# Kernel tuning notes

Measured on AMD Instinct MI355X. Metric: run time of the kernel, lower is better.

## Reference

```python
import jax, jax.numpy as jnp
import numpy as np

B, T, C = 2, 2048, 1024
N_HEAD, N_GROUP = 16, 4
N_KV = N_HEAD // N_GROUP          # 4
HEAD_DIM = C // N_HEAD            # 64
ROPE_BASE = 10000.0
INIT_STD = 0.02


def setup_inputs() -> dict:
    key = jax.random.key(0)
    ks = jax.random.split(key, 5)
    kvC = N_KV * HEAD_DIM
    return {
        "x": jax.random.normal(ks[0], (B, T, C), jnp.float32),
        "w_q": jax.random.normal(ks[1], (C, C), jnp.float32) * INIT_STD,
        "b_q": jnp.zeros((C,), jnp.float32),
        "w_k": jax.random.normal(ks[2], (C, kvC), jnp.float32) * INIT_STD,
        "b_k": jnp.zeros((kvC,), jnp.float32),
        "w_v": jax.random.normal(ks[3], (C, kvC), jnp.float32) * INIT_STD,
        "b_v": jnp.zeros((kvC,), jnp.float32),
        "w_o": jax.random.normal(ks[4], (C, C), jnp.float32) * INIT_STD,
        "b_o": jnp.zeros((C,), jnp.float32),
    }


def reference(x, w_q, b_q, w_k, b_k, w_v, b_v, w_o, b_o):
    Bx, Tx, Cx = x.shape
    # projections (torch Linear math with weights stored as [in, out])
    q = (x @ w_q + b_q).reshape(Bx, Tx, N_HEAD, HEAD_DIM).transpose(0, 2, 1, 3)  # [B,H,T,hd]
    k = (x @ w_k + b_k).reshape(Bx, Tx, N_KV, HEAD_DIM).transpose(0, 2, 1, 3)    # [B,KV,T,hd]
    v = (x @ w_v + b_v).reshape(Bx, Tx, N_KV, HEAD_DIM).transpose(0, 2, 1, 3)

    # RoPE with INTERLEAVED pair convention: pairs are (dim 2i, dim 2i+1)
    inv_freq = 1.0 / (ROPE_BASE ** (jnp.arange(0, HEAD_DIM, 2, dtype=jnp.float32) / HEAD_DIM))
    freqs = jnp.arange(Tx, dtype=jnp.float32)[:, None] * inv_freq[None, :]       # [T, hd/2]
    cos, sin = jnp.cos(freqs), jnp.sin(freqs)

    def rope(t):
        tp = t.reshape(*t.shape[:-1], HEAD_DIM // 2, 2)
        e, o = tp[..., 0], tp[..., 1]          # even/odd lanes, [B,h,T,hd/2]
        er = e * cos - o * sin
        orr = e * sin + o * cos
        return jnp.stack([er, orr], axis=-1).reshape(t.shape)

    q, k = rope(q), rope(k)

    # GQA: duplicate each KV head n_group times (consecutively, like repeat_interleave)
    k = jnp.repeat(k, N_GROUP, axis=1)   # [B,H,T,hd]
    v = jnp.repeat(v, N_GROUP, axis=1)

    attn = jnp.einsum('bhqd,bhkd->bhqk', q, k) / np.sqrt(HEAD_DIM).astype(np.float32)
    causal = jnp.tril(jnp.ones((Tx, Tx), bool))
    attn = jnp.where(causal, attn, -jnp.inf)
    attn = jax.nn.softmax(attn, axis=-1)

    out = jnp.einsum('bhqk,bhkd->bhqd', attn, v)            # [B,H,T,hd]
    out = out.transpose(0, 2, 1, 3).reshape(Bx, Tx, Cx)
    return out @ w_o + b_o
```

## Files before the change

kernel.cpp:

```cpp
#include <hip/hip_runtime.h>
#include <hip/hip_bf16.h>

typedef __hip_bfloat16 bf16;
typedef __attribute__((ext_vector_type(8))) short short8_t;
typedef __attribute__((ext_vector_type(4))) short short4_t;
typedef __attribute__((ext_vector_type(4))) float f32x4;

#define B_SZ   2
#define T_SEQ  2048
#define C_DIM  1024
#define NH     16
#define NKV    4
#define HD     64
#define QKVW   1536
#define MTOK   (B_SZ * T_SEQ)

#define LOG2_BASE_OVER_32 0.4152410118609203f
#define Q_SCALE 0.1803368801111204f

__device__ __forceinline__ short f2bs(float f) {
    unsigned u = __float_as_uint(f);
    u += 0x7FFFu + ((u >> 16) & 1u);
    return (short)(u >> 16);
}
__device__ __forceinline__ short f2bs_trunc(float f) {
    return (short)(__float_as_uint(f) >> 16);
}
__device__ __forceinline__ float bs2f(short s) {
    unsigned u = ((unsigned)(unsigned short)s) << 16;
    return __uint_as_float(u);
}
__device__ __forceinline__ float dpp_xor1(float x) {
    return __int_as_float(
        __builtin_amdgcn_update_dpp(0, __float_as_int(x), 0xB1, 0xF, 0xF, true));
}
__device__ __forceinline__ float fast_exp2(float x) {
    float r;
    asm("v_exp_f32 %0, %1" : "=v"(r) : "v"(x));
    return r;
}
__device__ __forceinline__ unsigned pack_bf16_trunc(float lo, float hi) {
    return __builtin_amdgcn_perm(__float_as_uint(hi), __float_as_uint(lo),
                                 0x07060302u);
}
__device__ __forceinline__ void gload_lds16(const short* g, short* l) {
    __builtin_amdgcn_global_load_lds(
        (const __attribute__((address_space(1))) void*)g,
        (__attribute__((address_space(3))) void*)l, 16, 0, 0);
}

__device__ __forceinline__ void transpose_tile(
    const float* __restrict__ W, short* __restrict__ Wt,
    int K, int N, int n0, int k0, int tid)
{
    __shared__ float tile[32][33];
    int tx = tid & 31, ty = tid >> 5;
    #pragma unroll
    for (int i = 0; i < 4; ++i)
        tile[ty + 8 * i][tx] = W[(size_t)(k0 + ty + 8 * i) * N + n0 + tx];
    __syncthreads();
    #pragma unroll
    for (int i = 0; i < 4; ++i)
        Wt[(size_t)(n0 + ty + 8 * i) * K + k0 + tx] = f2bs(tile[tx][ty + 8 * i]);
}

__global__ __launch_bounds__(256) void prep_kernel(
    const float* __restrict__ x,
    const float* __restrict__ w_q, const float* __restrict__ w_k,
    const float* __restrict__ w_v, const float* __restrict__ w_o,
    const float* __restrict__ b_q, const float* __restrict__ b_k,
    const float* __restrict__ b_v,
    short* __restrict__ Xb, short* __restrict__ Wqkv, short* __restrict__ Wto,
    float* __restrict__ Bqkv, float2* __restrict__ Tab)
{
    int blk = blockIdx.x, tid = threadIdx.x;
    if (blk < 4096) {
        int i = blk * 1024 + tid * 4;
        float4 v = *(const float4*)(x + i);
        short4_t o;
        o[0] = f2bs(v.x); o[1] = f2bs(v.y); o[2] = f2bs(v.z); o[3] = f2bs(v.w);
        *(short4_t*)(Xb + i) = o;
    } else if (blk < 5120) {
        int l = blk - 4096;
        transpose_tile(w_q, Wqkv, C_DIM, C_DIM, (l & 31) * 32, (l >> 5) * 32, tid);
    } else if (blk < 5376) {
        int l = blk - 5120;
        transpose_tile(w_k, Wqkv + (size_t)1024 * C_DIM, C_DIM, 256,
                       (l & 7) * 32, (l >> 3) * 32, tid);
    } else if (blk < 5632) {
        int l = blk - 5376;
        transpose_tile(w_v, Wqkv + (size_t)1280 * C_DIM, C_DIM, 256,
                       (l & 7) * 32, (l >> 3) * 32, tid);
    } else if (blk < 6656) {
        int l = blk - 5632;
        transpose_tile(w_o, Wto, C_DIM, C_DIM, (l & 31) * 32, (l >> 5) * 32, tid);
    } else if (blk < 6662) {
        int i = (blk - 6656) * 256 + tid;
        float v;
        if (i < 1024)      v = b_q[i];
        else if (i < 1280) v = b_k[i - 1024];
        else               v = b_v[i - 1280];
        Bqkv[i] = v;
    } else {
        int idx = (blk - 6662) * 256 + tid;
        int t = idx >> 5, i = idx & 31;
        float ang = (float)t * exp2f(-(float)i * LOG2_BASE_OVER_32);
        Tab[idx] = make_float2(cosf(ang), sinf(ang));
    }
}

#define GEMM_STAGE(dstA, dstB, Aptr, Bptr, k0)                                  \
    {                                                                           \
        _Pragma("unroll")                                                       \
        for (int it = 0; it < 4; ++it) {                                        \
            int i = (w * 4 + it) * 64 + lane;                                   \
            int row = i >> 3, p = i & 7;                                        \
            int gc = (k0) + ((p ^ (row & 7)) << 3);                             \
            gload_lds16((Aptr) + (size_t)(m0 + row) * K + gc,                   \
                        (dstA) + (w * 4 + it) * 512);                           \
        }                                                                       \
        _Pragma("unroll")                                                       \
        for (int it = 0; it < 4; ++it) {                                        \
            int i = (w * 4 + it) * 64 + lane;                                   \
            int row = i >> 3, p = i & 7;                                        \
            int gc = (k0) + ((p ^ (row & 7)) << 3);                             \
            gload_lds16((Bptr) + (size_t)(n0 + row) * K + gc,                   \
                        (dstB) + (w * 4 + it) * 512);                           \
        }                                                                       \
    }

#define GEMM_COMPUTE(srcA, srcB)                                                \
    {                                                                           \
        _Pragma("unroll")                                                       \
        for (int ks = 0; ks < 2; ++ks) {                                        \
            short8_t af[4], bf[4];                                              \
            _Pragma("unroll")                                                   \
            for (int mt = 0; mt < 4; ++mt) {                                    \
                int r = wm * 64 + mt * 16 + l16;                                \
                int g = ks * 4 + quad;                                          \
                af[mt] = *(const short8_t*)&(srcA)[r * 64 + ((g ^ (r & 7)) << 3)]; \
            }                                                                   \
            _Pragma("unroll")                                                   \
            for (int nt = 0; nt < 4; ++nt) {                                    \
                int r = wn * 64 + nt * 16 + l16;                                \
                int g = ks * 4 + quad;                                          \
                bf[nt] = *(const short8_t*)&(srcB)[r * 64 + ((g ^ (r & 7)) << 3)]; \
            }                                                                   \
            _Pragma("unroll")                                                   \
            for (int mt = 0; mt < 4; ++mt)                                      \
                _Pragma("unroll")                                               \
                for (int nt = 0; nt < 4; ++nt)                                  \
                    acc[mt][nt] = __builtin_amdgcn_mfma_f32_16x16x32_bf16(      \
                        af[mt], bf[nt], acc[mt][nt], 0, 0, 0);                  \
        }                                                                       \
    }

#define GEMM_KLOOP(Aptr, Bptr)                                                  \
    GEMM_STAGE(sA(0), sB(0), Aptr, Bptr, 0);                                    \
    for (int t = 0; t < NT; ++t) {                                              \
        int cur = t & 1;                                                        \
        if (t + 1 < NT) {                                                       \
            GEMM_STAGE(sA(cur ^ 1), sB(cur ^ 1), Aptr, Bptr, (t + 1) * 64);     \
            asm volatile("s_waitcnt vmcnt(8)" ::: "memory");                    \
        } else {                                                                \
            asm volatile("s_waitcnt vmcnt(0)" ::: "memory");                    \
        }                                                                       \
        __builtin_amdgcn_s_barrier();                                           \
        __builtin_amdgcn_sched_barrier(0);                                      \
        GEMM_COMPUTE(sA(cur), sB(cur));                                         \
        __builtin_amdgcn_sched_barrier(0);                                      \
        __builtin_amdgcn_s_barrier();                                           \
    }

__global__ __launch_bounds__(256) void gemm_qkv(
    const short* __restrict__ A, const short* __restrict__ Bt,
    const float* __restrict__ bias, const float2* __restrict__ Tab,
    short* __restrict__ QKVb, short* __restrict__ Vt)
{
    __shared__ __align__(16) short smem[32768];
    #define sA(b) (smem + (b) * 16384)
    #define sB(b) (smem + (b) * 16384 + 8192)

    const int K = C_DIM, NT = C_DIM / 64;
    int m0 = blockIdx.y * 128;
    int n0 = blockIdx.x * 128;
    int tid  = threadIdx.x;
    int w    = tid >> 6, lane = tid & 63;
    int quad = lane >> 4, l16 = lane & 15;
    int wm = w & 1, wn = w >> 1;

    f32x4 acc[4][4] = {};

    GEMM_KLOOP(A, Bt);

    if (n0 < 1280) {
        float scale = (n0 < 1024) ? Q_SCALE : 1.0f;
        float sgn   = (l16 & 1) ? 1.0f : -1.0f;
        #pragma unroll
        for (int nt = 0; nt < 4; ++nt) {
            int col = n0 + wn * 64 + nt * 16 + l16;
            int ip  = (col & 63) >> 1;
            float bv = bias[col];
            #pragma unroll
            for (int mt = 0; mt < 4; ++mt) {
                #pragma unroll
                for (int r = 0; r < 4; ++r) {
                    int row = m0 + wm * 64 + mt * 16 + quad * 4 + r;
                    float v = acc[mt][nt][r] + bv;
                    float po = dpp_xor1(v);
                    float2 cs = Tab[(row & (T_SEQ - 1)) * 32 + ip];
                    float res = (v * cs.x + sgn * po * cs.y) * scale;
                    QKVb[(size_t)row * QKVW + col] = f2bs(res);
                }
            }
        }
    } else {
        short (*sT)[136] = (short(*)[136])smem;
        #pragma unroll
        for (int h2 = 0; h2 < 2; ++h2) {
            if (wn == h2) {
                #pragma unroll
                for (int nt = 0; nt < 4; ++nt) {
                    int col_l = nt * 16 + l16;
                    float bv = bias[n0 + h2 * 64 + col_l];
                    #pragma unroll
                    for (int mt = 0; mt < 4; ++mt)
                        #pragma unroll
                        for (int r = 0; r < 4; ++r)
                            sT[col_l][wm * 64 + mt * 16 + quad * 4 + r] =
                                f2bs(acc[mt][nt][r] + bv);
                }
            }
            __syncthreads();
            int d0 = n0 - 1280 + h2 * 64;
            #pragma unroll
            for (int it = 0; it < 4; ++it) {
                int slot = tid + 256 * it;
                int dl = slot >> 4, seg = (slot & 15) * 8;
                *(short8_t*)(Vt + (size_t)(d0 + dl) * MTOK + m0 + seg) =
                    *(const short8_t*)&sT[dl][seg];
            }
            __syncthreads();
        }
    }
    #undef sA
    #undef sB
}

__global__ __launch_bounds__(256) void gemm_mfma_o(
    const short* __restrict__ A, const short* __restrict__ Bt,
    const float* __restrict__ bias, float* __restrict__ C,
    int M, int N, int K_, int unused)
{
    __shared__ __align__(16) short smem[32768];
    #define sA(b) (smem + (b) * 16384)
    #define sB(b) (smem + (b) * 16384 + 8192)

    const int K = C_DIM, NT = C_DIM / 64;
    int m0 = blockIdx.y * 128;
    int n0 = blockIdx.x * 128;
    int tid  = threadIdx.x;
    int w    = tid >> 6, lane = tid & 63;
    int quad = lane >> 4, l16 = lane & 15;
    int wm = w & 1, wn = w >> 1;

    f32x4 acc[4][4] = {};

    GEMM_KLOOP(A, Bt);

    #pragma unroll
    for (int mt = 0; mt < 4; ++mt) {
        #pragma unroll
        for (int nt = 0; nt < 4; ++nt) {
            int col = n0 + wn * 64 + nt * 16 + l16;
            float bv = bias[col];
            #pragma unroll
            for (int r = 0; r < 4; ++r) {
                int row = m0 + wm * 64 + mt * 16 + quad * 4 + r;
                C[(size_t)row * N + col] = acc[mt][nt][r] + bv;
            }
        }
    }
    #undef sA
    #undef sB
}

__global__ __launch_bounds__(512) void attn_mfma14(
    const short* __restrict__ QKV, const short* __restrict__ Vt,
    short* __restrict__ O)
{
    __shared__ __align__(16) short sK [2][64][64];
    __shared__ __align__(16) short sVt[2][64][72];

    const int tid  = threadIdx.x;
    const int w    = tid >> 6;
    const int lane = tid & 63;
    const int quad = lane >> 4;
    const int l16  = lane & 15;

    int blk = blockIdx.x;
    int grp = blk & 7;
    int pr  = 63 - (blk >> 3);
    int kvh = grp & 3;
    int b   = grp >> 2;
    int h   = kvh * 4 + (w & 3);
    int tq  = pr * 2 + (w >> 2);
    int ct  = pr >> 1;
    int tg  = tq * 16 + l16;

    const short* qptr = QKV + ((size_t)(b * T_SEQ) + tq * 16 + l16) * QKVW + h * HD;
    short8_t qf0 = *(const short8_t*)(qptr + quad * 8);
    short8_t qf1 = *(const short8_t*)(qptr + quad * 8 + 32);

    const short* kbase  = QKV + (size_t)b * T_SEQ * QKVW + 1024 + kvh * HD;
    const short* vtbase = Vt + (size_t)(kvh * HD) * MTOK + b * T_SEQ;

    float m_l = -INFINITY, l_l = 0.f;
    f32x4 oacc[4];
    #pragma unroll
    for (int dt = 0; dt < 4; ++dt) oacc[dt] = (f32x4){0.f, 0.f, 0.f, 0.f};

    const int kr_  = tid >> 3;
    const int kg   = tid & 7;
    const int ksrc = (kg ^ (kr_ & 7)) << 3;

    const int vdim = tid >> 3;
    const int s8   = tid & 7;
    const int vseg = s8 * 8;
    const int P0   = ((s8 & 4) << 3) | ((s8 & 1) << 4) | ((s8 & 2) << 1);

    const int c0g = quad ^ (l16 & 7);

    gload_lds16(kbase + (size_t)kr_ * QKVW + ksrc, (short*)sK[0] + (w << 9));
    {
        short8_t v0 = *(const short8_t*)(vtbase + (size_t)vdim * MTOK + vseg);
        union { short8_t v; short4_t h[2]; } u; u.v = v0;
        *(short4_t*)&sVt[0][vdim][P0]     = u.h[0];
        *(short4_t*)&sVt[0][vdim][P0 + 8] = u.h[1];
    }
    __syncthreads();

    short8_t vr;
    for (int c = 0; c <= ct; ++c) {
        const int buf = c & 1;

        if (c < ct) {
            int jn = (c + 1) * 64;
            gload_lds16(kbase + (size_t)(jn + kr_) * QKVW + ksrc,
                        (short*)sK[buf ^ 1] + (w << 9));
            vr = *(const short8_t*)(vtbase + (size_t)vdim * MTOK + jn + vseg);
        }

        f32x4 sacc[4];
        __builtin_amdgcn_s_setprio(1);
        #pragma unroll
        for (int kt = 0; kt < 4; ++kt) {
            f32x4 z = {0.f, 0.f, 0.f, 0.f};
            const short* krow = &sK[buf][l16 + 16 * kt][0];
            short8_t kf0 = *(const short8_t*)(krow + (c0g << 3));
            short8_t kf1 = *(const short8_t*)(krow + ((c0g ^ 4) << 3));
            z = __builtin_amdgcn_mfma_f32_16x16x32_bf16(kf0, qf0, z, 0, 0, 0);
            z = __builtin_amdgcn_mfma_f32_16x16x32_bf16(kf1, qf1, z, 0, 0, 0);
            sacc[kt] = z;
        }
        __builtin_amdgcn_s_setprio(0);

        short8_t vf0[4];
        #pragma unroll
        for (int dt = 0; dt < 4; ++dt)
            vf0[dt] = *(const short8_t*)&sVt[buf][16 * dt + l16][quad * 8];

        if (c == ct) {
            int j0 = c * 64;
            #pragma unroll
            for (int kt = 0; kt < 4; ++kt)
                #pragma unroll
                for (int r = 0; r < 4; ++r)
                    if (j0 + 16 * kt + quad * 4 + r > tg) sacc[kt][r] = -INFINITY;
        }

        float v0 = fmaxf(fmaxf(sacc[0][0], sacc[0][1]), fmaxf(sacc[0][2], sacc[0][3]));
        float v1 = fmaxf(fmaxf(sacc[1][0], sacc[1][1]), fmaxf(sacc[1][2], sacc[1][3]));
        float v2 = fmaxf(fmaxf(sacc[2][0], sacc[2][1]), fmaxf(sacc[2][2], sacc[2][3]));
        float v3 = fmaxf(fmaxf(sacc[3][0], sacc[3][1]), fmaxf(sacc[3][2], sacc[3][3]));
        float vloc = fmaxf(fmaxf(v0, v1), fmaxf(v2, v3));

        if (!__all(vloc <= m_l + 8.0f)) {
            float vmax = fmaxf(vloc, __shfl_xor(vloc, 16));
            vmax = fmaxf(vmax, __shfl_xor(vmax, 32));
            float mnew = fmaxf(m_l, vmax);
            float al = fast_exp2(m_l - mnew);
            m_l = mnew;
            l_l *= al;
            #pragma unroll
            for (int r = 0; r < 4; ++r) {
                float alr = __shfl(al, quad * 4 + r);
                #pragma unroll
                for (int dt = 0; dt < 4; ++dt) oacc[dt][r] *= alr;
            }
        }

        float psum = 0.f;
        unsigned pk0, pk1, pk2, pk3, pk4, pk5, pk6, pk7;
        {
            float p0 = fast_exp2(sacc[0][0] - m_l), p1 = fast_exp2(sacc[0][1] - m_l);
            float p2 = fast_exp2(sacc[0][2] - m_l), p3 = fast_exp2(sacc[0][3] - m_l);
            psum += (p0 + p1) + (p2 + p3);
            pk0 = pack_bf16_trunc(p0, p1); pk1 = pack_bf16_trunc(p2, p3);
        }
        {
            float p0 = fast_exp2(sacc[1][0] - m_l), p1 = fast_exp2(sacc[1][1] - m_l);
            float p2 = fast_exp2(sacc[1][2] - m_l), p3 = fast_exp2(sacc[1][3] - m_l);
            psum += (p0 + p1) + (p2 + p3);
            pk2 = pack_bf16_trunc(p0, p1); pk3 = pack_bf16_trunc(p2, p3);
        }
        {
            float p0 = fast_exp2(sacc[2][0] - m_l), p1 = fast_exp2(sacc[2][1] - m_l);
            float p2 = fast_exp2(sacc[2][2] - m_l), p3 = fast_exp2(sacc[2][3] - m_l);
            psum += (p0 + p1) + (p2 + p3);
            pk4 = pack_bf16_trunc(p0, p1); pk5 = pack_bf16_trunc(p2, p3);
        }
        {
            float p0 = fast_exp2(sacc[3][0] - m_l), p1 = fast_exp2(sacc[3][1] - m_l);
            float p2 = fast_exp2(sacc[3][2] - m_l), p3 = fast_exp2(sacc[3][3] - m_l);
            psum += (p0 + p1) + (p2 + p3);
            pk6 = pack_bf16_trunc(p0, p1); pk7 = pack_bf16_trunc(p2, p3);
        }
        l_l += psum;

        short8_t pf0, pf1;
        {
            union { unsigned u[4]; short8_t v; } fa, fb;
            fa.u[0] = pk0; fa.u[1] = pk1; fa.u[2] = pk2; fa.u[3] = pk3;
            fb.u[0] = pk4; fb.u[1] = pk5; fb.u[2] = pk6; fb.u[3] = pk7;
            pf0 = fa.v; pf1 = fb.v;
        }

        __builtin_amdgcn_s_setprio(1);
        #pragma unroll
        for (int dt = 0; dt < 4; ++dt) {
            short8_t vf1 = *(const short8_t*)&sVt[buf][16 * dt + l16][quad * 8 + 32];
            oacc[dt] = __builtin_amdgcn_mfma_f32_16x16x32_bf16(pf0, vf0[dt], oacc[dt], 0, 0, 0);
            oacc[dt] = __builtin_amdgcn_mfma_f32_16x16x32_bf16(pf1, vf1, oacc[dt], 0, 0, 0);
        }
        __builtin_amdgcn_s_setprio(0);

        if (c < ct) {
            union { short8_t v; short4_t h[2]; } u; u.v = vr;
            *(short4_t*)&sVt[buf ^ 1][vdim][P0]     = u.h[0];
            *(short4_t*)&sVt[buf ^ 1][vdim][P0 + 8] = u.h[1];
        }
        __syncthreads();
    }

    l_l += __shfl_xor(l_l, 16);
    l_l += __shfl_xor(l_l, 32);

    #pragma unroll
    for (int r = 0; r < 4; ++r) {
        int m = quad * 4 + r;
        float lr = __shfl(l_l, quad * 4 + r);
        float inv = __builtin_amdgcn_rcpf(lr);
        #pragma unroll
        for (int dt = 0; dt < 4; ++dt)
            O[((size_t)b * T_SEQ + tq * 16 + m) * C_DIM + h * HD + 16 * dt + l16] =
                f2bs(oacc[dt][r] * inv);
    }
}

extern "C" void kernel_launch(void* const* d_in, const int* in_sizes, int n_in,
                              void* d_out, int out_size, void* d_ws, size_t ws_size,
                              hipStream_t stream)
{
    const float* x   = (const float*)d_in[0];
    const float* w_q = (const float*)d_in[1];
    const float* b_q = (const float*)d_in[2];
    const float* w_k = (const float*)d_in[3];
    const float* b_k = (const float*)d_in[4];
    const float* w_v = (const float*)d_in[5];
    const float* b_v = (const float*)d_in[6];
    const float* w_o = (const float*)d_in[7];
    const float* b_o = (const float*)d_in[8];
    float* out = (float*)d_out;

    char* ws = (char*)d_ws;
    short*  Xb   = (short*) (ws);
    short*  Ab   = (short*) (ws + ((size_t)8  << 20));
    short*  QKVb = (short*) (ws + ((size_t)16 << 20));
    short*  Wqkv = (short*) (ws + ((size_t)28 << 20));
    short*  Wto  = (short*) (ws + ((size_t)31 << 20));
    float*  Bqkv = (float*) (ws + ((size_t)33 << 20));
    float2* Tab  = (float2*)(ws + ((size_t)33 << 20) + 8192);
    short*  Vt   = (short*) (ws + ((size_t)34 << 20));

    const int M = MTOK;

    prep_kernel<<<6918, 256, 0, stream>>>(
        x, w_q, w_k, w_v, w_o, b_q, b_k, b_v, Xb, Wqkv, Wto, Bqkv, Tab);

    gemm_qkv<<<dim3(QKVW / 128, M / 128), 256, 0, stream>>>(
        Xb, Wqkv, Bqkv, Tab, QKVb, Vt);

    attn_mfma14<<<B_SZ * NKV * 64, 512, 0, stream>>>(QKVb, Vt, Ab);

    gemm_mfma_o<<<dim3(C_DIM / 128, M / 128), 256, 0, stream>>>(
        Ab, Wto, b_o, out, M, C_DIM, C_DIM, 0);
}
```

Before: 162.7 us.

## Software-pipeline attention loop: compute next QK^T scores during current softmax/PV

Restructures the attention main loop so the QK^T scores for tile c+1 are computed before the softmax and PV of tile c, and K/V global loads are issued two tiles ahead. This lets MFMA work on the next scores overlap the exp/pack VALU work of the current tile and hides load latency. The barrier moves to the top of the loop and V fragment loads move inside the PV loop. It costs extra registers for the second score buffer, which may hurt occupancy, and the buffer reuse timing needs care to avoid races.

```diff
diff --git a/kernel.cpp b/kernel.cpp
--- a/kernel.cpp
+++ b/kernel.cpp
@@ -285,7 +285,7 @@
     #undef sB
 }
 
-__global__ __launch_bounds__(512) void attn_mfma14(
+__global__ __launch_bounds__(512) void attn_mfma15(
     const short* __restrict__ QKV, const short* __restrict__ Vt,
     short* __restrict__ O)
 {
@@ -338,37 +338,48 @@
         *(short4_t*)&sVt[0][vdim][P0]     = u.h[0];
         *(short4_t*)&sVt[0][vdim][P0 + 8] = u.h[1];
     }
+    short8_t vr;
+    if (ct > 0) {
+        gload_lds16(kbase + (size_t)(64 + kr_) * QKVW + ksrc,
+                    (short*)sK[1] + (w << 9));
+        vr = *(const short8_t*)(vtbase + (size_t)vdim * MTOK + 64 + vseg);
+    }
     __syncthreads();
 
-    short8_t vr;
+    f32x4 sacc[4], sacc_n[4];
+    #pragma unroll
+    for (int kt = 0; kt < 4; ++kt) {
+        f32x4 z = {0.f, 0.f, 0.f, 0.f};
+        const short* krow = &sK[0][l16 + 16 * kt][0];
+        short8_t kf0 = *(const short8_t*)(krow + (c0g << 3));
+        short8_t kf1 = *(const short8_t*)(krow + ((c0g ^ 4) << 3));
+        z = __builtin_amdgcn_mfma_f32_16x16x32_bf16(kf0, qf0, z, 0, 0, 0);
+        z = __builtin_amdgcn_mfma_f32_16x16x32_bf16(kf1, qf1, z, 0, 0, 0);
+        sacc[kt] = z;
+    }
+
     for (int c = 0; c <= ct; ++c) {
         const int buf = c & 1;
-
+        __syncthreads();
+
+        __builtin_amdgcn_s_setprio(1);
         if (c < ct) {
-            int jn = (c + 1) * 64;
-            gload_lds16(kbase + (size_t)(jn + kr_) * QKVW + ksrc,
-                        (short*)sK[buf ^ 1] + (w << 9));
-            vr = *(const short8_t*)(vtbase + (size_t)vdim * MTOK + jn + vseg);
-        }
-
-        f32x4 sacc[4];
-        __builtin_amdgcn_s_setprio(1);
-        #pragma unroll
-        for (int kt = 0; kt < 4; ++kt) {
-            f32x4 z = {0.f, 0.f, 0.f, 0.f};
-            const short* krow = &sK[buf][l16 + 16 * kt][0];
-            short8_t kf0 = *(const short8_t*)(krow + (c0g << 3));
-            short8_t kf1 = *(const short8_t*)(krow + ((c0g ^ 4) << 3));
-            z = __builtin_amdgcn_mfma_f32_16x16x32_bf16(kf0, qf0, z, 0, 0, 0);
-            z = __builtin_amdgcn_mfma_f32_16x16x32_bf16(kf1, qf1, z, 0, 0, 0);
-            sacc[kt] = z;
-        }
-        __builtin_amdgcn_s_setprio(0);
-
-        short8_t vf0[4];
-        #pragma unroll
-        for (int dt = 0; dt < 4; ++dt)
-            vf0[dt] = *(const short8_t*)&sVt[buf][16 * dt + l16][quad * 8];
+            #pragma unroll
+            for (int kt = 0; kt < 4; ++kt) {
+                f32x4 z = {0.f, 0.f, 0.f, 0.f};
+                const short* krow = &sK[buf ^ 1][l16 + 16 * kt][0];
+                short8_t kf0 = *(const short8_t*)(krow + (c0g << 3));
+                short8_t kf1 = *(const short8_t*)(krow + ((c0g ^ 4) << 3));
+                z = __builtin_amdgcn_mfma_f32_16x16x32_bf16(kf0, qf0, z, 0, 0, 0);
+                z = __builtin_amdgcn_mfma_f32_16x16x32_bf16(kf1, qf1, z, 0, 0, 0);
+                sacc_n[kt] = z;
+            }
+            if (c + 2 <= ct) {
+                int jn = (c + 2) * 64;
+                gload_lds16(kbase + (size_t)(jn + kr_) * QKVW + ksrc,
+                            (short*)sK[buf] + (w << 9));
+            }
+        }
 
         if (c == ct) {
             int j0 = c * 64;
@@ -436,21 +447,26 @@
             pf0 = fa.v; pf1 = fb.v;
         }
 
-        __builtin_amdgcn_s_setprio(1);
+        if (c < ct) {
+            union { short8_t v; short4_t hh[2]; } u; u.v = vr;
+            *(short4_t*)&sVt[buf ^ 1][vdim][P0]     = u.hh[0];
+            *(short4_t*)&sVt[buf ^ 1][vdim][P0 + 8] = u.hh[1];
+            if (c + 2 <= ct)
+                vr = *(const short8_t*)(vtbase + (size_t)vdim * MTOK
+                                        + (c + 2) * 64 + vseg);
+        }
+
         #pragma unroll
         for (int dt = 0; dt < 4; ++dt) {
+            short8_t vf0 = *(const short8_t*)&sVt[buf][16 * dt + l16][quad * 8];
             short8_t vf1 = *(const short8_t*)&sVt[buf][16 * dt + l16][quad * 8 + 32];
-            oacc[dt] = __builtin_amdgcn_mfma_f32_16x16x32_bf16(pf0, vf0[dt], oacc[dt], 0, 0, 0);
+            oacc[dt] = __builtin_amdgcn_mfma_f32_16x16x32_bf16(pf0, vf0, oacc[dt], 0, 0, 0);
             oacc[dt] = __builtin_amdgcn_mfma_f32_16x16x32_bf16(pf1, vf1, oacc[dt], 0, 0, 0);
         }
         __builtin_amdgcn_s_setprio(0);
 
-        if (c < ct) {
-            union { short8_t v; short4_t h[2]; } u; u.v = vr;
-            *(short4_t*)&sVt[buf ^ 1][vdim][P0]     = u.h[0];
-            *(short4_t*)&sVt[buf ^ 1][vdim][P0 + 8] = u.h[1];
-        }
-        __syncthreads();
+        #pragma unroll
+        for (int kt = 0; kt < 4; ++kt) sacc[kt] = sacc_n[kt];
     }
 
     l_l += __shfl_xor(l_l, 16);
@@ -501,7 +517,7 @@
     gemm_qkv<<<dim3(QKVW / 128, M / 128), 256, 0, stream>>>(
         Xb, Wqkv, Bqkv, Tab, QKVb, Vt);
 
-    attn_mfma14<<<B_SZ * NKV * 64, 512, 0, stream>>>(QKVb, Vt, Ab);
+    attn_mfma15<<<B_SZ * NKV * 64, 512, 0, stream>>>(QKVb, Vt, Ab);
 
     gemm_mfma_o<<<dim3(C_DIM / 128, M / 128), 256, 0, stream>>>(
         Ab, Wto, b_o, out, M, C_DIM, C_DIM, 0);
```

After: 159.6 us. No clear change (-1.9%).
